# Kernel tuning notes

Measured on AMD Instinct MI355X. Metric: run time of the kernel, lower is better.

Reference implementation:

```python
import jax, jax.numpy as jnp
import numpy as np
from jax import lax

LATENT = 100
B, D, H, W = 32768, 120, 4, 2
BN_EPS = 1e-5


def setup_inputs() -> dict:
    key = jax.random.key(0)
    ks = jax.random.split(key, 12)
    inp = {
        "x1": jax.random.normal(ks[0], (B, 1, D, H, W), dtype=jnp.float32),
        "x2": jax.random.normal(ks[1], (B, 1), dtype=jnp.float32),
        "shifts": jax.random.randint(ks[2], (B, 2), 0, 5),
        "nonzero_mask_xm": jax.random.randint(ks[3], (B, 1, D, H, W), 0, 2).astype(jnp.bool_),
        # conv3d_1 / conv3d_2: Conv3d(1,1,kernel=(7,3,1)) -> OIDHW weights
        "w1": jax.random.normal(ks[4], (1, 1, 7, 3, 1), dtype=jnp.float32) * 0.2,
        "b1": jax.random.normal(ks[5], (1,), dtype=jnp.float32) * 0.1,
        "w2": jax.random.normal(ks[6], (1, 1, 7, 3, 1), dtype=jnp.float32) * 0.2,
        "b2": jax.random.normal(ks[7], (1,), dtype=jnp.float32) * 0.1,
        "fcm1_w": jax.random.normal(ks[8], (10, 80), dtype=jnp.float32) * 0.1,
        "fcm1_b": jnp.zeros((10,), dtype=jnp.float32),
        "fc_w": jax.random.normal(ks[9], (LATENT, 11), dtype=jnp.float32) * 0.3,
        "fc_b": jnp.zeros((LATENT,), dtype=jnp.float32),
    }
    return inp


def conv3d(x, w, b, pad):
    y = lax.conv_general_dilated(
        x, w, window_strides=(1, 1, 1),
        padding=[(p, p) for p in pad],
        dimension_numbers=("NCDHW", "OIDHW", "NCDHW"))
    return y + b.reshape(1, -1, 1, 1, 1)


def maxpool_d(x, k):
    # MaxPool3d((k,1,1)) with return_indices; indices flat over (D,H,W) like torch
    b, c, d, h, w = x.shape
    xr = x.reshape(b, c, d // k, k, h, w)
    vals = xr.max(axis=3)
    off = xr.argmax(axis=3)  # [b,c,d//k,h,w]
    d_idx = jnp.arange(d // k).reshape(1, 1, -1, 1, 1) * k + off
    h_idx = jnp.arange(h).reshape(1, 1, 1, -1, 1)
    w_idx = jnp.arange(w).reshape(1, 1, 1, 1, -1)
    idx = (d_idx * h + h_idx) * w + w_idx
    return vals, idx


def reference(x1, x2, shifts, nonzero_mask_xm, w1, b1, w2, b2, fcm1_w, fcm1_b, fc_w, fc_b):
    # eval-mode forward: augmentation ops are identity, rand_shift is None
    aug_xm = x1
    xm, pool1_indices = maxpool_d(jax.nn.relu(conv3d(aug_xm, w1, b1, (3, 1, 0))), 4)
    xm, pool2_indices = maxpool_d(jax.nn.relu(conv3d(xm, w2, b2, (3, 1, 0))), 3)
    xm = xm.reshape(xm.shape[0], -1)                       # [B, 80]
    xm = jnp.where(xm @ fcm1_w.T + fcm1_b > 0,
                   xm @ fcm1_w.T + fcm1_b,
                   jnp.expm1(xm @ fcm1_w.T + fcm1_b))       # ELU, [B, 10]
    aug_x_sd = x2
    x_sd = jax.nn.sigmoid(aug_x_sd)                        # [B, 1]
    xm = jnp.concatenate((xm, x_sd), axis=1)               # [B, 11]
    y = xm @ fc_w.T + fc_b                                 # [B, LATENT]
    # BatchNorm1d eval with fresh running stats (mean=0, var=1), affine=False
    z = y / jnp.sqrt(jnp.float32(1.0) + BN_EPS)
    return z, aug_xm, aug_x_sd, pool1_indices, pool2_indices
```

## Files before the change

### kernel.cpp

```cpp
#include <hip/hip_runtime.h>
#include <math.h>

#define B_TOT 32768
#define NPB 4

#define RS1 132
#define W1S (4 * RS1)
#define ZROW (8 * RS1)
#define XS_SZ 1216

#define P_RS 37
#define F2_OFF 320
#define V11_OFF 400

typedef float vf4 __attribute__((ext_vector_type(4)));
typedef float vf2 __attribute__((ext_vector_type(2)));

__device__ __forceinline__ void wave_sync() {
    __builtin_amdgcn_s_waitcnt(0xC07F);
    __builtin_amdgcn_wave_barrier();
}

__global__ __launch_bounds__(256, 8) void encoder_kernel(
    const float* __restrict__ x1, const float* __restrict__ x2,
    const float* __restrict__ w1, const float* __restrict__ b1,
    const float* __restrict__ w2, const float* __restrict__ b2,
    const float* __restrict__ fcm1_w, const float* __restrict__ fcm1_b,
    const float* __restrict__ fc_w, const float* __restrict__ fc_b,
    float* __restrict__ out)
{
    __shared__ __align__(16) float xs[NPB][XS_SZ];

    const int tid  = threadIdx.x;
    const int wv   = tid >> 6, lane = tid & 63;
    const long b   = (long)blockIdx.x * NPB + wv;

    const size_t XM0 = (size_t)B_TOT * 100;
    const size_t SD0 = XM0 + (size_t)B_TOT * 960;
    const size_t P10 = SD0 + (size_t)B_TOT;
    const size_t P20 = P10 + (size_t)B_TOT * 240;

    float w1r[21], w2r[21];
    #pragma unroll
    for (int k = 0; k < 21; k++) { w1r[k] = w1[k]; w2r[k] = w2[k]; }
    const float bb1 = b1[0], bb2 = b2[0];

    {
        const vf4 z4 = (vf4){0.f, 0.f, 0.f, 0.f};
        vf4* xz = (vf4*)xs[wv];
        #pragma unroll
        for (int t = 0; t < 5; t++) { int i = lane + 64 * t; if (i < XS_SZ / 4) xz[i] = z4; }
    }
    wave_sync();

    {
        const vf4* xin = (const vf4*)(x1 + b * 960);
        vf4*       xo  = (vf4*)(out + XM0 + b * 960);
        #pragma unroll
        for (int t = 0; t < 4; t++) {
            int i = lane + 64 * t;
            if (i < 240) {
                vf4 v = xin[i];
                __builtin_nontemporal_store(v, &xo[i]);
                int bd = (i >> 1) + 3;
                int hb = 2 * (i & 1);
                xs[wv][ hb      * RS1       + bd] = v.x;
                xs[wv][ hb      * RS1 + W1S + bd] = v.y;
                xs[wv][(hb + 1) * RS1       + bd] = v.z;
                xs[wv][(hb + 1) * RS1 + W1S + bd] = v.w;
            }
        }
    }
    wave_sync();

    float pv[4];
    #pragma unroll
    for (int t = 0; t < 4; t++) {
        int p = lane + 64 * t;
        float best = 0.f;
        if (p < 240) {
            int dd = p >> 3, h = (p >> 1) & 3, w = p & 1;
            int d0 = 4 * dd;
            float va[3][10];
            #pragma unroll
            for (int kh = 0; kh < 3; kh++) {
                int r = h + kh - 1;
                int base = ((unsigned)r < 4u) ? (w * W1S + r * RS1 + d0) : (ZROW + d0);
                const float* bp = &xs[wv][base];
                vf4 q0 = *(const vf4*)bp;
                vf4 q1 = *(const vf4*)(bp + 4);
                vf2 q2 = *(const vf2*)(bp + 8);
                va[kh][0]=q0.x; va[kh][1]=q0.y; va[kh][2]=q0.z; va[kh][3]=q0.w;
                va[kh][4]=q1.x; va[kh][5]=q1.y; va[kh][6]=q1.z; va[kh][7]=q1.w;
                va[kh][8]=q2.x; va[kh][9]=q2.y;
            }
            int bj = 0;
            #pragma unroll
            for (int j = 0; j < 4; j++) {
                float acc = bb1;
                #pragma unroll
                for (int kd = 0; kd < 7; kd++)
                    #pragma unroll
                    for (int kh = 0; kh < 3; kh++)
                        acc = fmaf(va[kh][j + kd], w1r[kd * 3 + kh], acc);
                acc = fmaxf(acc, 0.f);
                if (j == 0)          { best = acc; }
                else if (acc > best) { best = acc; bj = j; }
            }
            __builtin_nontemporal_store(
                (float)(((dd * 4 + bj) * 4 + h) * 2 + w), &out[P10 + b * 240 + p]);
        }
        pv[t] = best;
    }
    wave_sync();

    if (lane < 48) {
        int row = lane / 6, pos = lane - row * 6;
        xs[wv][row * P_RS + (pos < 3 ? pos : pos + 30)] = 0.f;
    }
    #pragma unroll
    for (int t = 0; t < 4; t++) {
        int p = lane + 64 * t;
        if (p < 240) {
            int dd = p >> 3, h = (p >> 1) & 3, w = p & 1;
            xs[wv][(4 * w + h) * P_RS + dd + 3] = pv[t];
        }
    }
    wave_sync();

    #pragma unroll
    for (int t = 0; t < 2; t++) {
        int p = lane + 64 * t;
        if (p < 80) {
            int dd = p >> 3, h = (p >> 1) & 3, w = p & 1;
            int d0 = 3 * dd;
            float va[3][9];
            #pragma unroll
            for (int kh = 0; kh < 3; kh++) {
                int r = h + kh - 1;
                int base = ((unsigned)r < 4u) ? ((4 * w + r) * P_RS + d0) : (ZROW + d0);
                #pragma unroll
                for (int c = 0; c < 9; c++) va[kh][c] = xs[wv][base + c];
            }
            float best = 0.f; int bj = 0;
            #pragma unroll
            for (int j = 0; j < 3; j++) {
                float acc = bb2;
                #pragma unroll
                for (int kd = 0; kd < 7; kd++)
                    #pragma unroll
                    for (int kh = 0; kh < 3; kh++)
                        acc = fmaf(va[kh][j + kd], w2r[kd * 3 + kh], acc);
                acc = fmaxf(acc, 0.f);
                if (j == 0)          { best = acc; }
                else if (acc > best) { best = acc; bj = j; }
            }
            xs[wv][F2_OFF + p] = best;
            __builtin_nontemporal_store(
                (float)(((dd * 3 + bj) * 4 + h) * 2 + w), &out[P20 + b * 80 + p]);
        }
    }
    wave_sync();

    if (lane < 40) {
        int o = lane >> 2, q = lane & 3;
        const vf4* fp = (const vf4*)&xs[wv][F2_OFF + q * 20];
        const vf4* wp = (const vf4*)(fcm1_w + o * 80 + q * 20);
        float acc = 0.f;
        #pragma unroll
        for (int k = 0; k < 5; k++) {
            vf4 a = fp[k], c = wp[k];
            acc = fmaf(a.x, c.x, fmaf(a.y, c.y, fmaf(a.z, c.z, fmaf(a.w, c.w, acc))));
        }
        acc += __shfl_xor(acc, 1);
        acc += __shfl_xor(acc, 2);
        if (q == 0) {
            acc += fcm1_b[o];
            xs[wv][V11_OFF + o] = (acc > 0.f) ? acc : expm1f(acc);
        }
    } else if (lane == 40) {
        float xv = x2[b];
        xs[wv][V11_OFF + 10] = 1.f / (1.f + expf(-xv));
        __builtin_nontemporal_store(xv, &out[SD0 + b]);
    }
    wave_sync();

    {
        float fw0[11], fw1[11], fb0, fb1 = 0.f;
        #pragma unroll
        for (int k = 0; k < 11; k++) { fw0[k] = fc_w[lane * 11 + k]; fw1[k] = 0.f; }
        fb0 = fc_b[lane];
        if (lane < 36) {
            #pragma unroll
            for (int k = 0; k < 11; k++) fw1[k] = fc_w[(64 + lane) * 11 + k];
            fb1 = fc_b[64 + lane];
        }
        const float scale = 0.9999950000374997f;
        float vv[11];
        #pragma unroll
        for (int i = 0; i < 11; i++) vv[i] = xs[wv][V11_OFF + i];
        float a0 = fb0;
        #pragma unroll
        for (int i = 0; i < 11; i++) a0 = fmaf(vv[i], fw0[i], a0);
        __builtin_nontemporal_store(a0 * scale, &out[b * 100 + lane]);
        if (lane < 36) {
            float a1 = fb1;
            #pragma unroll
            for (int i = 0; i < 11; i++) a1 = fmaf(vv[i], fw1[i], a1);
            __builtin_nontemporal_store(a1 * scale, &out[b * 100 + 64 + lane]);
        }
    }
}

extern "C" void kernel_launch(void* const* d_in, const int* in_sizes, int n_in,
                              void* d_out, int out_size, void* d_ws, size_t ws_size,
                              hipStream_t stream) {
    const float* x1     = (const float*)d_in[0];
    const float* x2     = (const float*)d_in[1];
    const float* w1     = (const float*)d_in[4];
    const float* b1     = (const float*)d_in[5];
    const float* w2     = (const float*)d_in[6];
    const float* b2     = (const float*)d_in[7];
    const float* fcm1_w = (const float*)d_in[8];
    const float* fcm1_b = (const float*)d_in[9];
    const float* fc_w   = (const float*)d_in[10];
    const float* fc_b   = (const float*)d_in[11];
    float* out = (float*)d_out;

    dim3 grid(B_TOT / NPB), block(256);
    encoder_kernel<<<grid, block, 0, stream>>>(x1, x2, w1, b1, w2, b2,
                                               fcm1_w, fcm1_b, fc_w, fc_b, out);
}
```

Baseline: 340.1 us.

## Make encoder kernel persistent with register prefetch of next sample's input

Converts the one-sample-per-wave kernel into a persistent grid sized from occupancy, where each wave loops over samples with stride grid*4. The next sample's x1 row is loaded into registers while the current sample is being scattered and computed, so global load latency overlaps with compute. The conv inner loops are also reordered to keep four (or three) accumulators per row to expose ILP, and launch bounds drop to 6 blocks/SM to allow more registers. Risks include lower occupancy, extra register pressure from the prefetch buffers, and a hardcoded 256-CU assumption when sizing the grid.

```diff
diff --git a/kernel.cpp b/kernel.cpp
--- a/kernel.cpp
+++ b/kernel.cpp
@@ -21,7 +21,7 @@
     __builtin_amdgcn_wave_barrier();
 }
 
-__global__ __launch_bounds__(256, 8) void encoder_kernel(
+__global__ __launch_bounds__(256, 6) void encoder_kernel(
     const float* __restrict__ x1, const float* __restrict__ x2,
     const float* __restrict__ w1, const float* __restrict__ b1,
     const float* __restrict__ w2, const float* __restrict__ b2,
@@ -33,7 +33,8 @@
 
     const int tid  = threadIdx.x;
     const int wv   = tid >> 6, lane = tid & 63;
-    const long b   = (long)blockIdx.x * NPB + wv;
+    const int NW   = gridDim.x * NPB;
+    long b = (long)blockIdx.x * NPB + wv;
 
     const size_t XM0 = (size_t)B_TOT * 100;
     const size_t SD0 = XM0 + (size_t)B_TOT * 960;
@@ -45,170 +46,189 @@
     for (int k = 0; k < 21; k++) { w1r[k] = w1[k]; w2r[k] = w2[k]; }
     const float bb1 = b1[0], bb2 = b2[0];
 
-    {
-        const vf4 z4 = (vf4){0.f, 0.f, 0.f, 0.f};
-        vf4* xz = (vf4*)xs[wv];
-        #pragma unroll
-        for (int t = 0; t < 5; t++) { int i = lane + 64 * t; if (i < XS_SZ / 4) xz[i] = z4; }
-    }
-    wave_sync();
-
+    vf4 pf0 = (vf4){0,0,0,0}, pf1 = pf0, pf2 = pf0, pf3 = pf0;
     {
         const vf4* xin = (const vf4*)(x1 + b * 960);
-        vf4*       xo  = (vf4*)(out + XM0 + b * 960);
-        #pragma unroll
-        for (int t = 0; t < 4; t++) {
-            int i = lane + 64 * t;
-            if (i < 240) {
-                vf4 v = xin[i];
-                __builtin_nontemporal_store(v, &xo[i]);
+        pf0 = xin[lane]; pf1 = xin[lane + 64]; pf2 = xin[lane + 128];
+        if (lane < 48) pf3 = xin[lane + 192];
+    }
+
+    for (;;) {
+        const long nb = b + NW;
+
+        {
+            const vf4 z4 = (vf4){0.f, 0.f, 0.f, 0.f};
+            vf4* xz = (vf4*)xs[wv];
+            #pragma unroll
+            for (int t = 0; t < 5; t++) { int i = lane + 64 * t; if (i < XS_SZ / 4) xz[i] = z4; }
+        }
+
+        {
+            vf4* xo = (vf4*)(out + XM0 + b * 960);
+            __builtin_nontemporal_store(pf0, &xo[lane]);
+            __builtin_nontemporal_store(pf1, &xo[lane + 64]);
+            __builtin_nontemporal_store(pf2, &xo[lane + 128]);
+            if (lane < 48) __builtin_nontemporal_store(pf3, &xo[lane + 192]);
+
+            auto scat = [&](int i, vf4 v) {
                 int bd = (i >> 1) + 3;
                 int hb = 2 * (i & 1);
                 xs[wv][ hb      * RS1       + bd] = v.x;
                 xs[wv][ hb      * RS1 + W1S + bd] = v.y;
                 xs[wv][(hb + 1) * RS1       + bd] = v.z;
                 xs[wv][(hb + 1) * RS1 + W1S + bd] = v.w;
-            }
-        }
-    }
-    wave_sync();
-
-    float pv[4];
-    #pragma unroll
-    for (int t = 0; t < 4; t++) {
-        int p = lane + 64 * t;
-        float best = 0.f;
-        if (p < 240) {
-            int dd = p >> 3, h = (p >> 1) & 3, w = p & 1;
-            int d0 = 4 * dd;
-            float va[3][10];
-            #pragma unroll
-            for (int kh = 0; kh < 3; kh++) {
-                int r = h + kh - 1;
-                int base = ((unsigned)r < 4u) ? (w * W1S + r * RS1 + d0) : (ZROW + d0);
-                const float* bp = &xs[wv][base];
-                vf4 q0 = *(const vf4*)bp;
-                vf4 q1 = *(const vf4*)(bp + 4);
-                vf2 q2 = *(const vf2*)(bp + 8);
-                va[kh][0]=q0.x; va[kh][1]=q0.y; va[kh][2]=q0.z; va[kh][3]=q0.w;
-                va[kh][4]=q1.x; va[kh][5]=q1.y; va[kh][6]=q1.z; va[kh][7]=q1.w;
-                va[kh][8]=q2.x; va[kh][9]=q2.y;
-            }
-            int bj = 0;
-            #pragma unroll
-            for (int j = 0; j < 4; j++) {
-                float acc = bb1;
-                #pragma unroll
-                for (int kd = 0; kd < 7; kd++)
+            };
+            scat(lane,       pf0);
+            scat(lane + 64,  pf1);
+            scat(lane + 128, pf2);
+            if (lane < 48) scat(lane + 192, pf3);
+        }
+
+        if (nb < B_TOT) {
+            const vf4* xin = (const vf4*)(x1 + nb * 960);
+            pf0 = xin[lane]; pf1 = xin[lane + 64]; pf2 = xin[lane + 128];
+            if (lane < 48) pf3 = xin[lane + 192];
+        }
+        wave_sync();
+
+        float pv[4];
+        #pragma unroll
+        for (int t = 0; t < 4; t++) {
+            int p = lane + 64 * t;
+            float best = 0.f;
+            if (p < 240) {
+                int dd = p >> 3, h = (p >> 1) & 3, w = p & 1;
+                int d0 = 4 * dd;
+                float a0 = bb1, a1 = bb1, a2 = bb1, a3 = bb1;
+                #pragma unroll
+                for (int kh = 0; kh < 3; kh++) {
+                    int r = h + kh - 1;
+                    int base = ((unsigned)r < 4u) ? (w * W1S + r * RS1 + d0) : (ZROW + d0);
+                    const float* bp = &xs[wv][base];
+                    vf4 q0 = *(const vf4*)bp;
+                    vf4 q1 = *(const vf4*)(bp + 4);
+                    vf2 q2 = *(const vf2*)(bp + 8);
+                    float row[10] = {q0.x,q0.y,q0.z,q0.w,q1.x,q1.y,q1.z,q1.w,q2.x,q2.y};
                     #pragma unroll
-                    for (int kh = 0; kh < 3; kh++)
-                        acc = fmaf(va[kh][j + kd], w1r[kd * 3 + kh], acc);
-                acc = fmaxf(acc, 0.f);
-                if (j == 0)          { best = acc; }
-                else if (acc > best) { best = acc; bj = j; }
-            }
-            __builtin_nontemporal_store(
-                (float)(((dd * 4 + bj) * 4 + h) * 2 + w), &out[P10 + b * 240 + p]);
-        }
-        pv[t] = best;
-    }
-    wave_sync();
-
-    if (lane < 48) {
-        int row = lane / 6, pos = lane - row * 6;
-        xs[wv][row * P_RS + (pos < 3 ? pos : pos + 30)] = 0.f;
-    }
-    #pragma unroll
-    for (int t = 0; t < 4; t++) {
-        int p = lane + 64 * t;
-        if (p < 240) {
-            int dd = p >> 3, h = (p >> 1) & 3, w = p & 1;
-            xs[wv][(4 * w + h) * P_RS + dd + 3] = pv[t];
-        }
-    }
-    wave_sync();
-
-    #pragma unroll
-    for (int t = 0; t < 2; t++) {
-        int p = lane + 64 * t;
-        if (p < 80) {
-            int dd = p >> 3, h = (p >> 1) & 3, w = p & 1;
-            int d0 = 3 * dd;
-            float va[3][9];
-            #pragma unroll
-            for (int kh = 0; kh < 3; kh++) {
-                int r = h + kh - 1;
-                int base = ((unsigned)r < 4u) ? ((4 * w + r) * P_RS + d0) : (ZROW + d0);
-                #pragma unroll
-                for (int c = 0; c < 9; c++) va[kh][c] = xs[wv][base + c];
-            }
-            float best = 0.f; int bj = 0;
-            #pragma unroll
-            for (int j = 0; j < 3; j++) {
-                float acc = bb2;
-                #pragma unroll
-                for (int kd = 0; kd < 7; kd++)
+                    for (int kd = 0; kd < 7; kd++) {
+                        float wk = w1r[kd * 3 + kh];
+                        a0 = fmaf(row[kd],     wk, a0);
+                        a1 = fmaf(row[kd + 1], wk, a1);
+                        a2 = fmaf(row[kd + 2], wk, a2);
+                        a3 = fmaf(row[kd + 3], wk, a3);
+                    }
+                }
+                int bj = 0;
+                best = fmaxf(a0, 0.f);
+                float v1 = fmaxf(a1, 0.f); if (v1 > best) { best = v1; bj = 1; }
+                float v2 = fmaxf(a2, 0.f); if (v2 > best) { best = v2; bj = 2; }
+                float v3 = fmaxf(a3, 0.f); if (v3 > best) { best = v3; bj = 3; }
+                __builtin_nontemporal_store(
+                    (float)(((dd * 4 + bj) * 4 + h) * 2 + w), &out[P10 + b * 240 + p]);
+            }
+            pv[t] = best;
+        }
+        wave_sync();
+
+        if (lane < 48) {
+            int row = lane / 6, pos = lane - row * 6;
+            xs[wv][row * P_RS + (pos < 3 ? pos : pos + 30)] = 0.f;
+        }
+        #pragma unroll
+        for (int t = 0; t < 4; t++) {
+            int p = lane + 64 * t;
+            if (p < 240) {
+                int dd = p >> 3, h = (p >> 1) & 3, w = p & 1;
+                xs[wv][(4 * w + h) * P_RS + dd + 3] = pv[t];
+            }
+        }
+        wave_sync();
+
+        #pragma unroll
+        for (int t = 0; t < 2; t++) {
+            int p = lane + 64 * t;
+            if (p < 80) {
+                int dd = p >> 3, h = (p >> 1) & 3, w = p & 1;
+                int d0 = 3 * dd;
+                float a0 = bb2, a1 = bb2, a2 = bb2;
+                #pragma unroll
+                for (int kh = 0; kh < 3; kh++) {
+                    int r = h + kh - 1;
+                    int base = ((unsigned)r < 4u) ? ((4 * w + r) * P_RS + d0) : (ZROW + d0);
+                    float row[9];
                     #pragma unroll
-                    for (int kh = 0; kh < 3; kh++)
-                        acc = fmaf(va[kh][j + kd], w2r[kd * 3 + kh], acc);
-                acc = fmaxf(acc, 0.f);
-                if (j == 0)          { best = acc; }
-                else if (acc > best) { best = acc; bj = j; }
-            }
-            xs[wv][F2_OFF + p] = best;
-            __builtin_nontemporal_store(
-                (float)(((dd * 3 + bj) * 4 + h) * 2 + w), &out[P20 + b * 80 + p]);
-        }
-    }
-    wave_sync();
-
-    if (lane < 40) {
-        int o = lane >> 2, q = lane & 3;
-        const vf4* fp = (const vf4*)&xs[wv][F2_OFF + q * 20];
-        const vf4* wp = (const vf4*)(fcm1_w + o * 80 + q * 20);
-        float acc = 0.f;
-        #pragma unroll
-        for (int k = 0; k < 5; k++) {
-            vf4 a = fp[k], c = wp[k];
-            acc = fmaf(a.x, c.x, fmaf(a.y, c.y, fmaf(a.z, c.z, fmaf(a.w, c.w, acc))));
-        }
-        acc += __shfl_xor(acc, 1);
-        acc += __shfl_xor(acc, 2);
-        if (q == 0) {
-            acc += fcm1_b[o];
-            xs[wv][V11_OFF + o] = (acc > 0.f) ? acc : expm1f(acc);
-        }
-    } else if (lane == 40) {
-        float xv = x2[b];
-        xs[wv][V11_OFF + 10] = 1.f / (1.f + expf(-xv));
-        __builtin_nontemporal_store(xv, &out[SD0 + b]);
-    }
-    wave_sync();
-
-    {
-        float fw0[11], fw1[11], fb0, fb1 = 0.f;
-        #pragma unroll
-        for (int k = 0; k < 11; k++) { fw0[k] = fc_w[lane * 11 + k]; fw1[k] = 0.f; }
-        fb0 = fc_b[lane];
-        if (lane < 36) {
-            #pragma unroll
-            for (int k = 0; k < 11; k++) fw1[k] = fc_w[(64 + lane) * 11 + k];
-            fb1 = fc_b[64 + lane];
-        }
-        const float scale = 0.9999950000374997f;
-        float vv[11];
-        #pragma unroll
-        for (int i = 0; i < 11; i++) vv[i] = xs[wv][V11_OFF + i];
-        float a0 = fb0;
-        #pragma unroll
-        for (int i = 0; i < 11; i++) a0 = fmaf(vv[i], fw0[i], a0);
-        __builtin_nontemporal_store(a0 * scale, &out[b * 100 + lane]);
-        if (lane < 36) {
-            float a1 = fb1;
-            #pragma unroll
-            for (int i = 0; i < 11; i++) a1 = fmaf(vv[i], fw1[i], a1);
-            __builtin_nontemporal_store(a1 * scale, &out[b * 100 + 64 + lane]);
-        }
+                    for (int c = 0; c < 9; c++) row[c] = xs[wv][base + c];
+                    #pragma unroll
+                    for (int kd = 0; kd < 7; kd++) {
+                        float wk = w2r[kd * 3 + kh];
+                        a0 = fmaf(row[kd],     wk, a0);
+                        a1 = fmaf(row[kd + 1], wk, a1);
+                        a2 = fmaf(row[kd + 2], wk, a2);
+                    }
+                }
+                int bj = 0;
+                float best = fmaxf(a0, 0.f);
+                float v1 = fmaxf(a1, 0.f); if (v1 > best) { best = v1; bj = 1; }
+                float v2 = fmaxf(a2, 0.f); if (v2 > best) { best = v2; bj = 2; }
+                xs[wv][F2_OFF + p] = best;
+                __builtin_nontemporal_store(
+                    (float)(((dd * 3 + bj) * 4 + h) * 2 + w), &out[P20 + b * 80 + p]);
+            }
+        }
+        wave_sync();
+
+        if (lane < 40) {
+            int o = lane >> 2, q = lane & 3;
+            const vf4* fp = (const vf4*)&xs[wv][F2_OFF + q * 20];
+            const vf4* wp = (const vf4*)(fcm1_w + o * 80 + q * 20);
+            float acc = 0.f;
+            #pragma unroll
+            for (int k = 0; k < 5; k++) {
+                vf4 a = fp[k], c = wp[k];
+                acc = fmaf(a.x, c.x, fmaf(a.y, c.y, fmaf(a.z, c.z, fmaf(a.w, c.w, acc))));
+            }
+            acc += __shfl_xor(acc, 1);
+            acc += __shfl_xor(acc, 2);
+            if (q == 0) {
+                acc += fcm1_b[o];
+                xs[wv][V11_OFF + o] = (acc > 0.f) ? acc : expm1f(acc);
+            }
+        } else if (lane == 40) {
+            float xv = x2[b];
+            xs[wv][V11_OFF + 10] = 1.f / (1.f + expf(-xv));
+            __builtin_nontemporal_store(xv, &out[SD0 + b]);
+        }
+        wave_sync();
+
+        {
+            float fw0[11], fw1[11], fb0, fb1 = 0.f;
+            #pragma unroll
+            for (int k = 0; k < 11; k++) { fw0[k] = fc_w[lane * 11 + k]; fw1[k] = 0.f; }
+            fb0 = fc_b[lane];
+            if (lane < 36) {
+                #pragma unroll
+                for (int k = 0; k < 11; k++) fw1[k] = fc_w[(64 + lane) * 11 + k];
+                fb1 = fc_b[64 + lane];
+            }
+            const float scale = 0.9999950000374997f;
+            float vv[11];
+            #pragma unroll
+            for (int i = 0; i < 11; i++) vv[i] = xs[wv][V11_OFF + i];
+            float a0 = fb0;
+            #pragma unroll
+            for (int i = 0; i < 11; i++) a0 = fmaf(vv[i], fw0[i], a0);
+            __builtin_nontemporal_store(a0 * scale, &out[b * 100 + lane]);
+            if (lane < 36) {
+                float a1 = fb1;
+                #pragma unroll
+                for (int i = 0; i < 11; i++) a1 = fmaf(vv[i], fw1[i], a1);
+                __builtin_nontemporal_store(a1 * scale, &out[b * 100 + 64 + lane]);
+            }
+        }
+
+        b = nb;
+        if (b >= B_TOT) break;
+        wave_sync();
     }
 }
 
@@ -227,7 +247,18 @@
     const float* fc_b   = (const float*)d_in[11];
     float* out = (float*)d_out;
 
-    dim3 grid(B_TOT / NPB), block(256);
+    static int s_grid = 0;
+    if (s_grid == 0) {
+        int nb = 0;
+        if (hipOccupancyMaxActiveBlocksPerMultiprocessor(&nb, encoder_kernel, 256, 0)
+                != hipSuccess || nb < 1)
+            nb = 6;
+        long g = (long)nb * 256;
+        if (g > B_TOT / NPB) g = B_TOT / NPB;
+        s_grid = (int)g;
+    }
+
+    dim3 grid(s_grid), block(256);
     encoder_kernel<<<grid, block, 0, stream>>>(x1, x2, w1, b1, w2, b2,
                                                fcm1_w, fcm1_b, fc_w, fc_b, out);
 }
```

After: 497.3 us. 46.2% more time.

## Interleave W pair in LDS and compute convs with packed vf2 FMAs

Applied to the files above, without the earlier changes.

Reworks the shared-memory layout so each (d,h) row stores both W positions interleaved. Each thread then computes two W outputs at once with packed two-wide FMAs, using a rolling register window of loaded columns instead of reloading the full stencil. Pool-index outputs become vf2 stores. Nontemporal stores are replaced with regular stores. The aim is fewer LDS instructions and ALU ops per output, at the cost of a larger LDS tile per wave and some lanes idle in later stages.

```diff
diff --git a/kernel.cpp b/kernel.cpp
--- a/kernel.cpp
+++ b/kernel.cpp
@@ -4,17 +4,20 @@
 #define B_TOT 32768
 #define NPB 4
 
-#define RS1 132
-#define W1S (4 * RS1)
-#define ZROW (8 * RS1)
-#define XS_SZ 1216
-
-#define P_RS 37
-#define F2_OFF 320
-#define V11_OFF 400
+#define RS1 252
+#define ZR  1008
+#define TILE 1260
+
+#define PRS 72
+#define F2O 512
+#define V11O 600
 
 typedef float vf4 __attribute__((ext_vector_type(4)));
 typedef float vf2 __attribute__((ext_vector_type(2)));
+
+static __device__ __forceinline__ vf2 fma2(vf2 a, float w, vf2 c) {
+    return __builtin_elementwise_fma(a, (vf2){w, w}, c);
+}
 
 __device__ __forceinline__ void wave_sync() {
     __builtin_amdgcn_s_waitcnt(0xC07F);
@@ -29,7 +32,7 @@
     const float* __restrict__ fc_w, const float* __restrict__ fc_b,
     float* __restrict__ out)
 {
-    __shared__ __align__(16) float xs[NPB][XS_SZ];
+    __shared__ __align__(16) float xs[NPB][TILE];
 
     const int tid  = threadIdx.x;
     const int wv   = tid >> 6, lane = tid & 63;
@@ -49,7 +52,7 @@
         const vf4 z4 = (vf4){0.f, 0.f, 0.f, 0.f};
         vf4* xz = (vf4*)xs[wv];
         #pragma unroll
-        for (int t = 0; t < 5; t++) { int i = lane + 64 * t; if (i < XS_SZ / 4) xz[i] = z4; }
+        for (int t = 0; t < 5; t++) { int i = lane + 64 * t; if (i < TILE / 4) xz[i] = z4; }
     }
     wave_sync();
 
@@ -61,111 +64,140 @@
             int i = lane + 64 * t;
             if (i < 240) {
                 vf4 v = xin[i];
-                __builtin_nontemporal_store(v, &xo[i]);
-                int bd = (i >> 1) + 3;
-                int hb = 2 * (i & 1);
-                xs[wv][ hb      * RS1       + bd] = v.x;
-                xs[wv][ hb      * RS1 + W1S + bd] = v.y;
-                xs[wv][(hb + 1) * RS1       + bd] = v.z;
-                xs[wv][(hb + 1) * RS1 + W1S + bd] = v.w;
+                xo[i] = v;
+                int d  = i >> 1;
+                int h0 = 2 * (i & 1);
+                int fo = 2 * (d + 3);
+                *(vf2*)&xs[wv][ h0      * RS1 + fo] = (vf2){v.x, v.y};
+                *(vf2*)&xs[wv][(h0 + 1) * RS1 + fo] = (vf2){v.z, v.w};
             }
         }
     }
     wave_sync();
 
-    float pv[4];
-    #pragma unroll
-    for (int t = 0; t < 4; t++) {
-        int p = lane + 64 * t;
-        float best = 0.f;
-        if (p < 240) {
-            int dd = p >> 3, h = (p >> 1) & 3, w = p & 1;
-            int d0 = 4 * dd;
-            float va[3][10];
-            #pragma unroll
-            for (int kh = 0; kh < 3; kh++) {
-                int r = h + kh - 1;
-                int base = ((unsigned)r < 4u) ? (w * W1S + r * RS1 + d0) : (ZROW + d0);
-                const float* bp = &xs[wv][base];
-                vf4 q0 = *(const vf4*)bp;
-                vf4 q1 = *(const vf4*)(bp + 4);
-                vf2 q2 = *(const vf2*)(bp + 8);
-                va[kh][0]=q0.x; va[kh][1]=q0.y; va[kh][2]=q0.z; va[kh][3]=q0.w;
-                va[kh][4]=q1.x; va[kh][5]=q1.y; va[kh][6]=q1.z; va[kh][7]=q1.w;
-                va[kh][8]=q2.x; va[kh][9]=q2.y;
+    auto conv1_item = [&](int item) -> vf2 {
+        const int dd = item >> 2, h = item & 3;
+        const float* T = xs[wv];
+        int rb[3];
+        #pragma unroll
+        for (int kh = 0; kh < 3; kh++) {
+            int r = h + kh - 1;
+            rb[kh] = (((unsigned)r < 4u) ? r * RS1 : ZR) + 8 * dd;
+        }
+        vf2 A[3][4];
+        #pragma unroll
+        for (int kh = 0; kh < 3; kh++)
+            #pragma unroll
+            for (int p = 0; p < 4; p++)
+                A[kh][p] = *(const vf2*)&T[rb[kh] + 2 * p];
+        vf2 a0 = (vf2){bb1, bb1}, a1 = a0, a2 = a0, a3 = a0;
+        #pragma unroll
+        for (int kd = 0; kd < 7; kd++) {
+            const float wA = w1r[3 * kd], wB = w1r[3 * kd + 1], wC = w1r[3 * kd + 2];
+            a0 = fma2(A[0][ kd      & 3], wA, a0);
+            a0 = fma2(A[1][ kd      & 3], wB, a0);
+            a0 = fma2(A[2][ kd      & 3], wC, a0);
+            a1 = fma2(A[0][(kd + 1) & 3], wA, a1);
+            a1 = fma2(A[1][(kd + 1) & 3], wB, a1);
+            a1 = fma2(A[2][(kd + 1) & 3], wC, a1);
+            a2 = fma2(A[0][(kd + 2) & 3], wA, a2);
+            a2 = fma2(A[1][(kd + 2) & 3], wB, a2);
+            a2 = fma2(A[2][(kd + 2) & 3], wC, a2);
+            a3 = fma2(A[0][(kd + 3) & 3], wA, a3);
+            a3 = fma2(A[1][(kd + 3) & 3], wB, a3);
+            a3 = fma2(A[2][(kd + 3) & 3], wC, a3);
+            if (kd < 6) {
+                #pragma unroll
+                for (int kh = 0; kh < 3; kh++)
+                    A[kh][kd & 3] = *(const vf2*)&T[rb[kh] + 2 * (kd + 4)];
             }
-            int bj = 0;
-            #pragma unroll
-            for (int j = 0; j < 4; j++) {
-                float acc = bb1;
+        }
+        float bv0 = fmaxf(a0.x, 0.f); int j0 = 0;
+        float q;
+        q = fmaxf(a1.x, 0.f); if (q > bv0) { bv0 = q; j0 = 1; }
+        q = fmaxf(a2.x, 0.f); if (q > bv0) { bv0 = q; j0 = 2; }
+        q = fmaxf(a3.x, 0.f); if (q > bv0) { bv0 = q; j0 = 3; }
+        float bv1 = fmaxf(a0.y, 0.f); int j1 = 0;
+        q = fmaxf(a1.y, 0.f); if (q > bv1) { bv1 = q; j1 = 1; }
+        q = fmaxf(a2.y, 0.f); if (q > bv1) { bv1 = q; j1 = 2; }
+        q = fmaxf(a3.y, 0.f); if (q > bv1) { bv1 = q; j1 = 3; }
+        vf2 ix = {(float)(((dd * 4 + j0) * 4 + h) * 2),
+                  (float)(((dd * 4 + j1) * 4 + h) * 2 + 1)};
+        *(vf2*)&out[P10 + b * 240 + (size_t)item * 2] = ix;
+        return (vf2){bv0, bv1};
+    };
+    vf2 bp0 = conv1_item(lane);
+    vf2 bp1 = (vf2){0.f, 0.f};
+    if (lane < 56) bp1 = conv1_item(64 + lane);
+    wave_sync();
+
+    if (lane < 48) {
+        int row = lane / 12, pos = lane - row * 12;
+        xs[wv][row * PRS + (pos < 6 ? pos : pos + 60)] = 0.f;
+    }
+    {
+        int it0 = lane;
+        *(vf2*)&xs[wv][(it0 & 3) * PRS + 2 * ((it0 >> 2) + 3)] = bp0;
+        if (lane < 56) {
+            int it1 = 64 + lane;
+            *(vf2*)&xs[wv][(it1 & 3) * PRS + 2 * ((it1 >> 2) + 3)] = bp1;
+        }
+    }
+    wave_sync();
+
+    if (lane < 40) {
+        const int item = lane, dd = item >> 2, h = item & 3;
+        const float* T = xs[wv];
+        int rb[3];
+        #pragma unroll
+        for (int kh = 0; kh < 3; kh++) {
+            int r = h + kh - 1;
+            rb[kh] = (((unsigned)r < 4u) ? r * PRS : ZR) + 6 * dd;
+        }
+        vf2 A[3][3];
+        #pragma unroll
+        for (int kh = 0; kh < 3; kh++)
+            #pragma unroll
+            for (int p = 0; p < 3; p++)
+                A[kh][p] = *(const vf2*)&T[rb[kh] + 2 * p];
+        vf2 a0 = (vf2){bb2, bb2}, a1 = a0, a2 = a0;
+        #pragma unroll
+        for (int kd = 0; kd < 7; kd++) {
+            const float wA = w2r[3 * kd], wB = w2r[3 * kd + 1], wC = w2r[3 * kd + 2];
+            int s0 = kd % 3, s1 = (kd + 1) % 3, s2 = (kd + 2) % 3;
+            a0 = fma2(A[0][s0], wA, a0);
+            a0 = fma2(A[1][s0], wB, a0);
+            a0 = fma2(A[2][s0], wC, a0);
+            a1 = fma2(A[0][s1], wA, a1);
+            a1 = fma2(A[1][s1], wB, a1);
+            a1 = fma2(A[2][s1], wC, a1);
+            a2 = fma2(A[0][s2], wA, a2);
+            a2 = fma2(A[1][s2], wB, a2);
+            a2 = fma2(A[2][s2], wC, a2);
+            if (kd < 6) {
                 #pragma unroll
-                for (int kd = 0; kd < 7; kd++)
-                    #pragma unroll
-                    for (int kh = 0; kh < 3; kh++)
-                        acc = fmaf(va[kh][j + kd], w1r[kd * 3 + kh], acc);
-                acc = fmaxf(acc, 0.f);
-                if (j == 0)          { best = acc; }
-                else if (acc > best) { best = acc; bj = j; }
+                for (int kh = 0; kh < 3; kh++)
+                    A[kh][kd % 3] = *(const vf2*)&T[rb[kh] + 2 * (kd + 3)];
             }
-            __builtin_nontemporal_store(
-                (float)(((dd * 4 + bj) * 4 + h) * 2 + w), &out[P10 + b * 240 + p]);
-        }
-        pv[t] = best;
-    }
-    wave_sync();
-
-    if (lane < 48) {
-        int row = lane / 6, pos = lane - row * 6;
-        xs[wv][row * P_RS + (pos < 3 ? pos : pos + 30)] = 0.f;
-    }
-    #pragma unroll
-    for (int t = 0; t < 4; t++) {
-        int p = lane + 64 * t;
-        if (p < 240) {
-            int dd = p >> 3, h = (p >> 1) & 3, w = p & 1;
-            xs[wv][(4 * w + h) * P_RS + dd + 3] = pv[t];
-        }
-    }
-    wave_sync();
-
-    #pragma unroll
-    for (int t = 0; t < 2; t++) {
-        int p = lane + 64 * t;
-        if (p < 80) {
-            int dd = p >> 3, h = (p >> 1) & 3, w = p & 1;
-            int d0 = 3 * dd;
-            float va[3][9];
-            #pragma unroll
-            for (int kh = 0; kh < 3; kh++) {
-                int r = h + kh - 1;
-                int base = ((unsigned)r < 4u) ? ((4 * w + r) * P_RS + d0) : (ZROW + d0);
-                #pragma unroll
-                for (int c = 0; c < 9; c++) va[kh][c] = xs[wv][base + c];
-            }
-            float best = 0.f; int bj = 0;
-            #pragma unroll
-            for (int j = 0; j < 3; j++) {
-                float acc = bb2;
-                #pragma unroll
-                for (int kd = 0; kd < 7; kd++)
-                    #pragma unroll
-                    for (int kh = 0; kh < 3; kh++)
-                        acc = fmaf(va[kh][j + kd], w2r[kd * 3 + kh], acc);
-                acc = fmaxf(acc, 0.f);
-                if (j == 0)          { best = acc; }
-                else if (acc > best) { best = acc; bj = j; }
-            }
-            xs[wv][F2_OFF + p] = best;
-            __builtin_nontemporal_store(
-                (float)(((dd * 3 + bj) * 4 + h) * 2 + w), &out[P20 + b * 80 + p]);
-        }
+        }
+        float bv0 = fmaxf(a0.x, 0.f); int j0 = 0;
+        float q;
+        q = fmaxf(a1.x, 0.f); if (q > bv0) { bv0 = q; j0 = 1; }
+        q = fmaxf(a2.x, 0.f); if (q > bv0) { bv0 = q; j0 = 2; }
+        float bv1 = fmaxf(a0.y, 0.f); int j1 = 0;
+        q = fmaxf(a1.y, 0.f); if (q > bv1) { bv1 = q; j1 = 1; }
+        q = fmaxf(a2.y, 0.f); if (q > bv1) { bv1 = q; j1 = 2; }
+        *(vf2*)&xs[wv][F2O + item * 2] = (vf2){bv0, bv1};
+        vf2 ix = {(float)(((dd * 3 + j0) * 4 + h) * 2),
+                  (float)(((dd * 3 + j1) * 4 + h) * 2 + 1)};
+        *(vf2*)&out[P20 + b * 80 + (size_t)item * 2] = ix;
     }
     wave_sync();
 
     if (lane < 40) {
-        int o = lane >> 2, q = lane & 3;
-        const vf4* fp = (const vf4*)&xs[wv][F2_OFF + q * 20];
-        const vf4* wp = (const vf4*)(fcm1_w + o * 80 + q * 20);
+        int o = lane >> 2, q4 = lane & 3;
+        const vf4* fp = (const vf4*)&xs[wv][F2O + q4 * 20];
+        const vf4* wp = (const vf4*)(fcm1_w + o * 80 + q4 * 20);
         float acc = 0.f;
         #pragma unroll
         for (int k = 0; k < 5; k++) {
@@ -174,14 +206,14 @@
         }
         acc += __shfl_xor(acc, 1);
         acc += __shfl_xor(acc, 2);
-        if (q == 0) {
+        if (q4 == 0) {
             acc += fcm1_b[o];
-            xs[wv][V11_OFF + o] = (acc > 0.f) ? acc : expm1f(acc);
+            xs[wv][V11O + o] = (acc > 0.f) ? acc : expm1f(acc);
         }
     } else if (lane == 40) {
         float xv = x2[b];
-        xs[wv][V11_OFF + 10] = 1.f / (1.f + expf(-xv));
-        __builtin_nontemporal_store(xv, &out[SD0 + b]);
+        xs[wv][V11O + 10] = 1.f / (1.f + expf(-xv));
+        out[SD0 + b] = xv;
     }
     wave_sync();
 
@@ -198,16 +230,16 @@
         const float scale = 0.9999950000374997f;
         float vv[11];
         #pragma unroll
-        for (int i = 0; i < 11; i++) vv[i] = xs[wv][V11_OFF + i];
+        for (int i = 0; i < 11; i++) vv[i] = xs[wv][V11O + i];
         float a0 = fb0;
         #pragma unroll
         for (int i = 0; i < 11; i++) a0 = fmaf(vv[i], fw0[i], a0);
-        __builtin_nontemporal_store(a0 * scale, &out[b * 100 + lane]);
+        out[b * 100 + lane] = a0 * scale;
         if (lane < 36) {
             float a1 = fb1;
             #pragma unroll
             for (int i = 0; i < 11; i++) a1 = fmaf(vv[i], fw1[i], a1);
-            __builtin_nontemporal_store(a1 * scale, &out[b * 100 + 64 + lane]);
+            out[b * 100 + 64 + lane] = a1 * scale;
         }
     }
 }
```

After: 354.1 us. +4.1%, slower.
